# Kernel tuning notes

Measured on AMD Instinct MI355X. Metric: run time of the kernel, lower is better.

Reference implementation:

```python
import jax, jax.numpy as jnp
import numpy as np

EPS_RMS = 1.1920929e-07  # torch.finfo(float32).eps, RMSNorm default when eps=None
EPS_BN = 1e-5            # BatchNorm1d default eps
NUM_CODES = 4096
EMBED_DIM = 64


def rms_norm(x):
    # nn.RMSNorm(embed_dim, elementwise_affine=False)
    ms = jnp.mean(x * x, axis=-1, keepdims=True)
    return x * jax.lax.rsqrt(ms + EPS_RMS)


def get_codebook(codebook_weight, bn_weight, bn_bias):
    # BatchNorm1d with track_running_stats=False: batch stats over codebook rows
    mean = jnp.mean(codebook_weight, axis=0)
    var = jnp.var(codebook_weight, axis=0)  # biased variance, as torch BN uses
    h = (codebook_weight - mean) * jax.lax.rsqrt(var + EPS_BN) * bn_weight + bn_bias
    return rms_norm(h)


def setup_inputs() -> dict:
    key = jax.random.key(0)
    k1, k2 = jax.random.split(key)
    z = jax.random.normal(k1, (8, 4096, EMBED_DIM), dtype=jnp.float32)
    # codebook init: uniform(-1/num_codes, 1/num_codes)
    codebook_weight = jax.random.uniform(
        k2, (NUM_CODES, EMBED_DIM), dtype=jnp.float32,
        minval=-1.0 / NUM_CODES, maxval=1.0 / NUM_CODES)
    bn_weight = jnp.ones((EMBED_DIM,), dtype=jnp.float32)
    bn_bias = jnp.zeros((EMBED_DIM,), dtype=jnp.float32)
    return {"z": z, "codebook_weight": codebook_weight,
            "bn_weight": bn_weight, "bn_bias": bn_bias}


def reference(z, codebook_weight, bn_weight, bn_bias):
    # c_in / c_out are Identity since width == embed_dim
    z_e = rms_norm(z)                                   # [B, S, D]
    cb = get_codebook(codebook_weight, bn_weight, bn_bias)  # [K, D]

    z_flat = z_e.reshape(-1, z_e.shape[-1])             # [N, D]
    # argmin of cdist == argmin of squared distance (sqrt is monotone)
    d2 = (jnp.sum(z_flat * z_flat, axis=1, keepdims=True)
          - 2.0 * (z_flat @ cb.T)
          + jnp.sum(cb * cb, axis=1))                   # [N, K]
    q = jnp.argmin(d2, axis=1)                          # [N]

    z_q = cb[q].reshape(z_e.shape)                      # gather codes
    q = q.reshape(z_e.shape[:-1])

    # straight-through: gradient flows to z_e only
    z_q_st = z_e + jax.lax.stop_gradient(z_q - z_e)
    # ret_dict entries: 'z' (detached z_e), 'q', 'z_q' (detached)
    return (z_q_st, jax.lax.stop_gradient(z_e), q, jax.lax.stop_gradient(z_q))
```

## Files before the change

### kernel.cpp

```cpp
#include <hip/hip_runtime.h>
#include <math.h>

#define NROWS 32768
#define DIM   64
#define NCODE 4096
#define EPS_RMS 1.1920929e-07f
#define EPS_BN  1e-5f

typedef _Float16 f16x8 __attribute__((ext_vector_type(8)));
typedef float    f32x4 __attribute__((ext_vector_type(4)));

#define WS_PS   0
#define WS_PQ   16384
#define WS_CC   32768
#define WS_CB32 49152
#define WS_PH   (49152 + 1048576)
#define WS_PL   (WS_PH + 524288)

#define OUT1 ((size_t)NROWS * DIM)
#define OUT2 ((size_t)2 * NROWS * DIM)
#define OUT3 (OUT2 + NROWS)

#define MFMA16(a, b, c) __builtin_amdgcn_mfma_f32_16x16x32_f16(a, b, c, 0, 0, 0)

__global__ __launch_bounds__(256) void k_bn1(const float* __restrict__ w,
                                             char* __restrict__ wsb) {
    __shared__ float s1[4][64], s2[4][64];
    int lane = threadIdx.x & 63, v = threadIdx.x >> 6;
    long base = (long)blockIdx.x * 64 + v * 16;
    float s = 0.f, sq = 0.f;
    #pragma unroll
    for (int i = 0; i < 16; i++) {
        float x = w[(base + i) * DIM + lane];
        s += x; sq += x * x;
    }
    s1[v][lane] = s; s2[v][lane] = sq;
    __syncthreads();
    if (threadIdx.x < 64) {
        float ts = s1[0][lane] + s1[1][lane] + s1[2][lane] + s1[3][lane];
        float tq = s2[0][lane] + s2[1][lane] + s2[2][lane] + s2[3][lane];
        ((float*)(wsb + WS_PS))[blockIdx.x * 64 + lane] = ts;
        ((float*)(wsb + WS_PQ))[blockIdx.x * 64 + lane] = tq;
    }
}

__global__ __launch_bounds__(256) void k_cb(const float* __restrict__ w,
                                            const float* __restrict__ bnw,
                                            const float* __restrict__ bnb,
                                            char* __restrict__ wsb) {
    __shared__ float s1[4][64], s2[4][64], af[64], bf[64];
    __shared__ _Float16 sh[16][64], sl[16][64];
    int t = threadIdx.x, lane = t & 63, v = t >> 6;
    const float* ps = (const float*)(wsb + WS_PS);
    const float* pq = (const float*)(wsb + WS_PQ);
    float s = 0.f, sq = 0.f;
    #pragma unroll
    for (int b = 0; b < 16; b++) {
        s  += ps[(v * 16 + b) * 64 + lane];
        sq += pq[(v * 16 + b) * 64 + lane];
    }
    s1[v][lane] = s; s2[v][lane] = sq;
    __syncthreads();
    if (t < 64) {
        float ts = s1[0][lane] + s1[1][lane] + s1[2][lane] + s1[3][lane];
        float tq = s2[0][lane] + s2[1][lane] + s2[2][lane] + s2[3][lane];
        float mean = ts * (1.0f / NCODE);
        float var  = tq * (1.0f / NCODE) - mean * mean;
        float a = rsqrtf(var + EPS_BN) * bnw[lane];
        af[lane] = a;
        bf[lane] = bnb[lane] - mean * a;
    }
    __syncthreads();
    float a = af[lane], bb = bf[lane];
    float* cb32 = (float*)(wsb + WS_CB32);
    float* ccp  = (float*)(wsb + WS_CC);
    int g = blockIdx.x;
    #pragma unroll
    for (int i = 0; i < 4; i++) {
        int  rl  = v * 4 + i;
        long row = (long)g * 16 + rl;
        float x = w[row * DIM + lane];
        float h = fmaf(x, a, bb);
        float ss = h * h;
        #pragma unroll
        for (int m = 1; m < 64; m <<= 1) ss += __shfl_xor(ss, m);
        float rms = rsqrtf(ss * (1.0f / DIM) + EPS_RMS);
        float c = h * rms;
        cb32[row * DIM + lane] = c;
        _Float16 ch = (_Float16)c;
        sh[rl][lane] = ch;
        sl[rl][lane] = (_Float16)(c - (float)ch);
        float cs = c * c;
        #pragma unroll
        for (int m = 1; m < 64; m <<= 1) cs += __shfl_xor(cs, m);
        if (lane == 0) ccp[row] = -0.5f * cs;
    }
    __syncthreads();
    {
        int u = t & 127;
        int c = u >> 6, l = u & 63;
        int codel = l & 15;
        int kbase = c * 32 + (l >> 4) * 8;
        size_t dst = (size_t)((g * 2 + c) * 64 + l) * 16;
        if (t < 128) {
            *(f16x8*)(wsb + WS_PH + dst) = *(const f16x8*)&sh[codel][kbase];
        } else {
            *(f16x8*)(wsb + WS_PL + dst) = *(const f16x8*)&sl[codel][kbase];
        }
    }
}

__global__ __launch_bounds__(256, 3) void k_main(const float* __restrict__ z,
                                                 const char* __restrict__ wsb,
                                                 float* __restrict__ out) {
    __shared__ __align__(16) unsigned char sm[18688];

    const int tid  = threadIdx.x;
    const int lane = tid & 63;
    const int w    = tid >> 6;
    const int l15  = lane & 15;
    const int l4   = lane >> 4;
    const long rowbase = (long)blockIdx.x * 64;

    const float* ccnG = (const float*)(wsb + WS_CC);
    const float* cb32 = (const float*)(wsb + WS_CB32);

    {
        int r = tid >> 2, seg = tid & 3;
        const float4* zp = (const float4*)(z + (rowbase + r) * DIM + seg * 16);
        float4 v4[4];
        float ss = 0.f;
        #pragma unroll
        for (int i = 0; i < 4; i++) {
            v4[i] = zp[i];
            ss += v4[i].x * v4[i].x + v4[i].y * v4[i].y + v4[i].z * v4[i].z + v4[i].w * v4[i].w;
        }
        ss += __shfl_xor(ss, 1);
        ss += __shfl_xor(ss, 2);
        float rms = rsqrtf(ss * (1.0f / DIM) + EPS_RMS);
        float4* oz = (float4*)(out + OUT1 + (rowbase + r) * DIM + seg * 16);
        __align__(16) _Float16 hb[16], lb[16];
        #pragma unroll
        for (int i = 0; i < 4; i++) {
            float xs[4] = {v4[i].x, v4[i].y, v4[i].z, v4[i].w};
            #pragma unroll
            for (int j = 0; j < 4; j++) {
                float x = xs[j] * rms;
                _Float16 h = (_Float16)x;
                hb[i * 4 + j] = h;
                lb[i * 4 + j] = (_Float16)(x - (float)h);
                xs[j] = x;
            }
            oz[i] = make_float4(xs[0], xs[1], xs[2], xs[3]);
        }
        unsigned char* zhp = sm + r * 128 + seg * 32;
        ((f16x8*)zhp)[0] = ((f16x8*)hb)[0];
        ((f16x8*)zhp)[1] = ((f16x8*)hb)[1];
        unsigned char* zlp = zhp + 8192;
        ((f16x8*)zlp)[0] = ((f16x8*)lb)[0];
        ((f16x8*)zlp)[1] = ((f16x8*)lb)[1];
    }
    __syncthreads();

    f16x8 ah[4][2], al[4][2];
    #pragma unroll
    for (int s = 0; s < 4; s++)
        #pragma unroll
        for (int c = 0; c < 2; c++) {
            int off = (s * 16 + l15) * 128 + c * 64 + l4 * 16;
            ah[s][c] = *(const f16x8*)(sm + off);
            al[s][c] = *(const f16x8*)(sm + 8192 + off);
        }

    float bmax[4][4];
    int   bix[4][4];
    #pragma unroll
    for (int s = 0; s < 4; s++)
        #pragma unroll
        for (int r = 0; r < 4; r++) { bmax[s][r] = -3.4e38f; bix[s][r] = 0; }

    const int gw = w * 64;
    const char* pH = wsb + WS_PH + (size_t)(gw * 2) * 1024 + lane * 16;
    const char* pL = wsb + WS_PL + (size_t)(gw * 2) * 1024 + lane * 16;
    const float* cn = ccnG + gw * 16 + l15;

    #define LOADB(H0, H1, L0, L1, CC, k)                       \
        H0 = *(const f16x8*)(pH + (size_t)(k) * 2048);         \
        H1 = *(const f16x8*)(pH + (size_t)(k) * 2048 + 1024);  \
        L0 = *(const f16x8*)(pL + (size_t)(k) * 2048);         \
        L1 = *(const f16x8*)(pL + (size_t)(k) * 2048 + 1024);  \
        CC = cn[(k) * 16];

    #define COMPUTE(H0, H1, L0, L1, CC, k)                                        \
    {                                                                             \
        int code = (gw + (k)) * 16 + l15;                                         \
        _Pragma("unroll")                                                         \
        for (int s = 0; s < 4; s++) {                                             \
            f32x4 a2 = {CC, CC, CC, CC};                                          \
            a2 = MFMA16(ah[s][0], H0, a2);                                        \
            a2 = MFMA16(ah[s][1], H1, a2);                                        \
            a2 = MFMA16(ah[s][0], L0, a2);                                        \
            a2 = MFMA16(ah[s][1], L1, a2);                                        \
            a2 = MFMA16(al[s][0], H0, a2);                                        \
            a2 = MFMA16(al[s][1], H1, a2);                                        \
            _Pragma("unroll")                                                     \
            for (int r = 0; r < 4; r++) {                                         \
                if (a2[r] > bmax[s][r]) { bmax[s][r] = a2[r]; bix[s][r] = code; } \
            }                                                                     \
        }                                                                         \
    }

    f16x8 hA0, hA1, lA0, lA1, hB0, hB1, lB0, lB1;
    float ccA, ccB;
    LOADB(hA0, hA1, lA0, lA1, ccA, 0);
    #pragma unroll 1
    for (int k = 0; k < 62; k += 2) {
        LOADB(hB0, hB1, lB0, lB1, ccB, k + 1);
        COMPUTE(hA0, hA1, lA0, lA1, ccA, k);
        LOADB(hA0, hA1, lA0, lA1, ccA, k + 2);
        COMPUTE(hB0, hB1, lB0, lB1, ccB, k + 1);
    }
    LOADB(hB0, hB1, lB0, lB1, ccB, 63);
    COMPUTE(hA0, hA1, lA0, lA1, ccA, 62);
    COMPUTE(hB0, hB1, lB0, lB1, ccB, 63);

    float* redd = (float*)(sm + 16384);
    int*   redi = (int*)(sm + 17408);
    int*   bidx = (int*)(sm + 18432);
    #pragma unroll
    for (int s = 0; s < 4; s++)
        #pragma unroll
        for (int r = 0; r < 4; r++) {
            float d = bmax[s][r];
            int   ix = bix[s][r];
            #pragma unroll
            for (int m = 1; m < 16; m <<= 1) {
                float od = __shfl_xor(d, m);
                int   oi = __shfl_xor(ix, m);
                if (od > d || (od == d && oi < ix)) { d = od; ix = oi; }
            }
            if (l15 == 0) {
                int row = s * 16 + l4 * 4 + r;
                redd[row * 4 + w] = d;
                redi[row * 4 + w] = ix;
            }
        }
    __syncthreads();
    if (tid < 64) {
        float bv = redd[tid * 4];
        int   bi_ = redi[tid * 4];
        #pragma unroll
        for (int j = 1; j < 4; j++) {
            float dj = redd[tid * 4 + j];
            int   ij = redi[tid * 4 + j];
            if (dj > bv || (dj == bv && ij < bi_)) { bv = dj; bi_ = ij; }
        }
        bidx[tid] = bi_;
        out[OUT2 + rowbase + tid] = (float)bi_;
    }
    __syncthreads();
    {
        int r = tid >> 2, seg = tid & 3;
        int ix = bidx[r];
        const float4* src = (const float4*)(cb32 + (long)ix * DIM + seg * 16);
        float4* o0 = (float4*)(out + (rowbase + r) * DIM + seg * 16);
        float4* o3 = (float4*)(out + OUT3 + (rowbase + r) * DIM + seg * 16);
        #pragma unroll
        for (int i = 0; i < 4; i++) { float4 t4 = src[i]; o0[i] = t4; o3[i] = t4; }
    }
}

extern "C" void kernel_launch(void* const* d_in, const int* in_sizes, int n_in,
                              void* d_out, int out_size, void* d_ws, size_t ws_size,
                              hipStream_t stream) {
    const float* z   = (const float*)d_in[0];
    const float* w   = (const float*)d_in[1];
    const float* bnw = (const float*)d_in[2];
    const float* bnb = (const float*)d_in[3];
    float* out = (float*)d_out;
    char*  wsb = (char*)d_ws;

    k_bn1 <<<64,  256, 0, stream>>>(w, wsb);
    k_cb  <<<256, 256, 0, stream>>>(w, bnw, bnb, wsb);
    k_main<<<512, 256, 0, stream>>>(z, wsb, out);
}
```

Measured before the change: 70.26 us.

## Split codebook search across two blocks per row tile and merge in final kernel

The main kernel now launches twice as many blocks, and each block scans half of the codebook for its 64 rows. It writes per-row partial best score and index to workspace, and a new k_final kernel merges the two halves, gathers the code vectors and writes the outputs. Launch bounds raise the occupancy target from 3 to 4 blocks per CU. The aim is more parallelism across 256 CUs, at the cost of computing the z normalization twice, an extra kernel launch and a workspace round-trip.

```diff
diff --git a/kernel.cpp b/kernel.cpp
--- a/kernel.cpp
+++ b/kernel.cpp
@@ -16,6 +16,7 @@
 #define WS_CB32 49152
 #define WS_PH   (49152 + 1048576)
 #define WS_PL   (WS_PH + 524288)
+#define WS_PART (WS_PL + 524288)
 
 #define OUT1 ((size_t)NROWS * DIM)
 #define OUT2 ((size_t)2 * NROWS * DIM)
@@ -110,20 +111,21 @@
     }
 }
 
-__global__ __launch_bounds__(256, 3) void k_main(const float* __restrict__ z,
-                                                 const char* __restrict__ wsb,
+__global__ __launch_bounds__(256, 4) void k_main(const float* __restrict__ z,
+                                                 char* __restrict__ wsb,
                                                  float* __restrict__ out) {
-    __shared__ __align__(16) unsigned char sm[18688];
+    __shared__ __align__(16) unsigned char sm[18432];
 
     const int tid  = threadIdx.x;
     const int lane = tid & 63;
     const int w    = tid >> 6;
     const int l15  = lane & 15;
     const int l4   = lane >> 4;
-    const long rowbase = (long)blockIdx.x * 64;
+    const int rowblk = blockIdx.x >> 1;
+    const int half   = blockIdx.x & 1;
+    const long rowbase = (long)rowblk * 64;
 
     const float* ccnG = (const float*)(wsb + WS_CC);
-    const float* cb32 = (const float*)(wsb + WS_CB32);
 
     {
         int r = tid >> 2, seg = tid & 3;
@@ -151,7 +153,7 @@
                 lb[i * 4 + j] = (_Float16)(x - (float)h);
                 xs[j] = x;
             }
-            oz[i] = make_float4(xs[0], xs[1], xs[2], xs[3]);
+            if (half == 0) oz[i] = make_float4(xs[0], xs[1], xs[2], xs[3]);
         }
         unsigned char* zhp = sm + r * 128 + seg * 32;
         ((f16x8*)zhp)[0] = ((f16x8*)hb)[0];
@@ -179,7 +181,7 @@
         #pragma unroll
         for (int r = 0; r < 4; r++) { bmax[s][r] = -3.4e38f; bix[s][r] = 0; }
 
-    const int gw = w * 64;
+    const int gw = half * 128 + w * 32;
     const char* pH = wsb + WS_PH + (size_t)(gw * 2) * 1024 + lane * 16;
     const char* pL = wsb + WS_PL + (size_t)(gw * 2) * 1024 + lane * 16;
     const float* cn = ccnG + gw * 16 + l15;
@@ -214,19 +216,18 @@
     float ccA, ccB;
     LOADB(hA0, hA1, lA0, lA1, ccA, 0);
     #pragma unroll 1
-    for (int k = 0; k < 62; k += 2) {
+    for (int k = 0; k < 30; k += 2) {
         LOADB(hB0, hB1, lB0, lB1, ccB, k + 1);
         COMPUTE(hA0, hA1, lA0, lA1, ccA, k);
         LOADB(hA0, hA1, lA0, lA1, ccA, k + 2);
         COMPUTE(hB0, hB1, lB0, lB1, ccB, k + 1);
     }
-    LOADB(hB0, hB1, lB0, lB1, ccB, 63);
-    COMPUTE(hA0, hA1, lA0, lA1, ccA, 62);
-    COMPUTE(hB0, hB1, lB0, lB1, ccB, 63);
+    LOADB(hB0, hB1, lB0, lB1, ccB, 31);
+    COMPUTE(hA0, hA1, lA0, lA1, ccA, 30);
+    COMPUTE(hB0, hB1, lB0, lB1, ccB, 31);
 
     float* redd = (float*)(sm + 16384);
     int*   redi = (int*)(sm + 17408);
-    int*   bidx = (int*)(sm + 18432);
     #pragma unroll
     for (int s = 0; s < 4; s++)
         #pragma unroll
@@ -255,19 +256,30 @@
             int   ij = redi[tid * 4 + j];
             if (dj > bv || (dj == bv && ij < bi_)) { bv = dj; bi_ = ij; }
         }
-        bidx[tid] = bi_;
-        out[OUT2 + rowbase + tid] = (float)bi_;
-    }
-    __syncthreads();
-    {
-        int r = tid >> 2, seg = tid & 3;
-        int ix = bidx[r];
-        const float4* src = (const float4*)(cb32 + (long)ix * DIM + seg * 16);
-        float4* o0 = (float4*)(out + (rowbase + r) * DIM + seg * 16);
-        float4* o3 = (float4*)(out + OUT3 + (rowbase + r) * DIM + seg * 16);
-        #pragma unroll
-        for (int i = 0; i < 4; i++) { float4 t4 = src[i]; o0[i] = t4; o3[i] = t4; }
-    }
+        float* part = (float*)(wsb + WS_PART);
+        size_t off = ((size_t)half * NROWS + rowbase + tid) * 2;
+        part[off]     = bv;
+        part[off + 1] = (float)bi_;
+    }
+}
+
+__global__ __launch_bounds__(256) void k_final(const char* __restrict__ wsb,
+                                               float* __restrict__ out) {
+    int gid = blockIdx.x * 256 + threadIdx.x;
+    int r   = gid >> 3;
+    int seg = gid & 7;
+    const float* part = (const float*)(wsb + WS_PART);
+    const float* cb32 = (const float*)(wsb + WS_CB32);
+    float d0 = part[(size_t)r * 2],           i0f = part[(size_t)r * 2 + 1];
+    float d1 = part[((size_t)NROWS + r) * 2], i1f = part[((size_t)NROWS + r) * 2 + 1];
+    int i0 = (int)i0f, i1 = (int)i1f;
+    int best = (d1 > d0 || (d1 == d0 && i1 < i0)) ? i1 : i0;
+    const float4* src = (const float4*)(cb32 + (long)best * DIM + seg * 8);
+    float4* o0 = (float4*)(out + (size_t)r * DIM + seg * 8);
+    float4* o3 = (float4*)(out + OUT3 + (size_t)r * DIM + seg * 8);
+    #pragma unroll
+    for (int i = 0; i < 2; i++) { float4 t4 = src[i]; o0[i] = t4; o3[i] = t4; }
+    if (seg == 0) out[OUT2 + r] = (float)best;
 }
 
 extern "C" void kernel_launch(void* const* d_in, const int* in_sizes, int n_in,
@@ -280,7 +292,8 @@
     float* out = (float*)d_out;
     char*  wsb = (char*)d_ws;
 
-    k_bn1 <<<64,  256, 0, stream>>>(w, wsb);
-    k_cb  <<<256, 256, 0, stream>>>(w, bnw, bnb, wsb);
-    k_main<<<512, 256, 0, stream>>>(z, wsb, out);
-}
+    k_bn1  <<<64,   256, 0, stream>>>(w, wsb);
+    k_cb   <<<256,  256, 0, stream>>>(w, bnw, bnb, wsb);
+    k_main <<<1024, 256, 0, stream>>>(z, wsb, out);
+    k_final<<<NROWS * 8 / 256, 256, 0, stream>>>(wsb, out);
+}
```

New measurement: 209.8 us. 199% more time.

## Stage codebook tiles in LDS via async global_load_lds with double buffering

Applied to the files above, without the earlier changes.

Each block now handles 128 rows with 512 threads instead of 64 rows with 256 threads. The packed fp16 hi/lo codebook is streamed through a double-buffered LDS ring using global_load_lds. Each 128-code chunk is shared by all 8 waves, which split the work into 4 row groups by 2 code halves, instead of every wave streaming its own codes from global/L2 directly. This aims to cut redundant codebook traffic. In exchange it uses 96KB of LDS and adds a barrier per chunk, which limits occupancy and adds sync overhead.

```diff
diff --git a/kernel.cpp b/kernel.cpp
--- a/kernel.cpp
+++ b/kernel.cpp
@@ -22,6 +22,12 @@
 #define OUT3 (OUT2 + NROWS)
 
 #define MFMA16(a, b, c) __builtin_amdgcn_mfma_f32_16x16x32_f16(a, b, c, 0, 0, 0)
+
+__device__ __forceinline__ void gload16(void* lds, const void* g) {
+    __builtin_amdgcn_global_load_lds(
+        (const __attribute__((address_space(1))) unsigned int*)g,
+        (__attribute__((address_space(3))) unsigned int*)lds, 16, 0, 0);
+}
 
 __global__ __launch_bounds__(256) void k_bn1(const float* __restrict__ w,
                                              char* __restrict__ wsb) {
@@ -110,20 +116,37 @@
     }
 }
 
-__global__ __launch_bounds__(256, 3) void k_main(const float* __restrict__ z,
-                                                 const char* __restrict__ wsb,
+__global__ __launch_bounds__(512, 2) void k_main(const float* __restrict__ z,
+                                                 char* __restrict__ wsb,
                                                  float* __restrict__ out) {
-    __shared__ __align__(16) unsigned char sm[18688];
+    __shared__ __align__(16) unsigned char sm[98304];
 
     const int tid  = threadIdx.x;
     const int lane = tid & 63;
     const int w    = tid >> 6;
+    const int rg   = w & 3;
+    const int ch   = w >> 2;
     const int l15  = lane & 15;
     const int l4   = lane >> 4;
-    const long rowbase = (long)blockIdx.x * 64;
+    const long rowbase = (long)blockIdx.x * 128;
 
     const float* ccnG = (const float*)(wsb + WS_CC);
     const float* cb32 = (const float*)(wsb + WS_CB32);
+
+    const char* pH = wsb + WS_PH + w * 1024 + lane * 16;
+    const char* pL = wsb + WS_PL + w * 1024 + lane * 16;
+
+    #define STAGE(p, bufoff)                                                \
+    {                                                                       \
+        const char* gh = pH + (size_t)(p) * 16384;                          \
+        const char* gl = pL + (size_t)(p) * 16384;                          \
+        gload16(sm + (bufoff) + w * 1024,          gh);                     \
+        gload16(sm + (bufoff) + 8192 + w * 1024,   gh + 8192);              \
+        gload16(sm + (bufoff) + 16384 + w * 1024,  gl);                     \
+        gload16(sm + (bufoff) + 24576 + w * 1024,  gl + 8192);              \
+    }
+
+    STAGE(0, 0);
 
     {
         int r = tid >> 2, seg = tid & 3;
@@ -153,82 +176,89 @@
             }
             oz[i] = make_float4(xs[0], xs[1], xs[2], xs[3]);
         }
-        unsigned char* zhp = sm + r * 128 + seg * 32;
+        unsigned char* zhp = sm + 65536 + r * 128 + seg * 32;
         ((f16x8*)zhp)[0] = ((f16x8*)hb)[0];
         ((f16x8*)zhp)[1] = ((f16x8*)hb)[1];
-        unsigned char* zlp = zhp + 8192;
+        unsigned char* zlp = zhp + 16384;
         ((f16x8*)zlp)[0] = ((f16x8*)lb)[0];
         ((f16x8*)zlp)[1] = ((f16x8*)lb)[1];
     }
     __syncthreads();
 
-    f16x8 ah[4][2], al[4][2];
-    #pragma unroll
-    for (int s = 0; s < 4; s++)
+    f16x8 ah[2][2], al[2][2];
+    #pragma unroll
+    for (int s = 0; s < 2; s++)
         #pragma unroll
         for (int c = 0; c < 2; c++) {
-            int off = (s * 16 + l15) * 128 + c * 64 + l4 * 16;
+            int off = 65536 + (rg * 32 + s * 16 + l15) * 128 + c * 64 + l4 * 16;
             ah[s][c] = *(const f16x8*)(sm + off);
-            al[s][c] = *(const f16x8*)(sm + 8192 + off);
-        }
-
-    float bmax[4][4];
-    int   bix[4][4];
-    #pragma unroll
-    for (int s = 0; s < 4; s++)
+            al[s][c] = *(const f16x8*)(sm + 16384 + off);
+        }
+
+    float bmax[2][4];
+    int   bix[2][4];
+    #pragma unroll
+    for (int s = 0; s < 2; s++)
         #pragma unroll
         for (int r = 0; r < 4; r++) { bmax[s][r] = -3.4e38f; bix[s][r] = 0; }
 
-    const int gw = w * 64;
-    const char* pH = wsb + WS_PH + (size_t)(gw * 2) * 1024 + lane * 16;
-    const char* pL = wsb + WS_PL + (size_t)(gw * 2) * 1024 + lane * 16;
-    const float* cn = ccnG + gw * 16 + l15;
-
-    #define LOADB(H0, H1, L0, L1, CC, k)                       \
-        H0 = *(const f16x8*)(pH + (size_t)(k) * 2048);         \
-        H1 = *(const f16x8*)(pH + (size_t)(k) * 2048 + 1024);  \
-        L0 = *(const f16x8*)(pL + (size_t)(k) * 2048);         \
-        L1 = *(const f16x8*)(pL + (size_t)(k) * 2048 + 1024);  \
-        CC = cn[(k) * 16];
-
-    #define COMPUTE(H0, H1, L0, L1, CC, k)                                        \
-    {                                                                             \
-        int code = (gw + (k)) * 16 + l15;                                         \
-        _Pragma("unroll")                                                         \
-        for (int s = 0; s < 4; s++) {                                             \
-            f32x4 a2 = {CC, CC, CC, CC};                                          \
-            a2 = MFMA16(ah[s][0], H0, a2);                                        \
-            a2 = MFMA16(ah[s][1], H1, a2);                                        \
-            a2 = MFMA16(ah[s][0], L0, a2);                                        \
-            a2 = MFMA16(ah[s][1], L1, a2);                                        \
-            a2 = MFMA16(al[s][0], H0, a2);                                        \
-            a2 = MFMA16(al[s][1], H1, a2);                                        \
-            _Pragma("unroll")                                                     \
-            for (int r = 0; r < 4; r++) {                                         \
-                if (a2[r] > bmax[s][r]) { bmax[s][r] = a2[r]; bix[s][r] = code; } \
-            }                                                                     \
-        }                                                                         \
-    }
-
-    f16x8 hA0, hA1, lA0, lA1, hB0, hB1, lB0, lB1;
-    float ccA, ccB;
-    LOADB(hA0, hA1, lA0, lA1, ccA, 0);
+    float ccv[4];
+    #pragma unroll
+    for (int q = 0; q < 4; q++)
+        ccv[q] = ccnG[ch * 64 + q * 16 + l15];
+
+    #define COMPUTE(p, bufoff)                                                     \
+    {                                                                              \
+        _Pragma("unroll")                                                          \
+        for (int q = 0; q < 4; q++) {                                              \
+            f16x8 bh[2], bl[2];                                                    \
+            _Pragma("unroll")                                                      \
+            for (int c = 0; c < 2; c++) {                                          \
+                int boff = (bufoff) + (ch * 8 + q * 2 + c) * 1024 + lane * 16;     \
+                bh[c] = *(const f16x8*)(sm + boff);                                \
+                bl[c] = *(const f16x8*)(sm + 16384 + boff);                        \
+            }                                                                      \
+            int code = (p) * 128 + ch * 64 + q * 16 + l15;                         \
+            _Pragma("unroll")                                                      \
+            for (int s = 0; s < 2; s++) {                                          \
+                f32x4 a2 = {ccv[q], ccv[q], ccv[q], ccv[q]};                       \
+                a2 = MFMA16(ah[s][0], bh[0], a2);                                  \
+                a2 = MFMA16(ah[s][1], bh[1], a2);                                  \
+                a2 = MFMA16(ah[s][0], bl[0], a2);                                  \
+                a2 = MFMA16(ah[s][1], bl[1], a2);                                  \
+                a2 = MFMA16(al[s][0], bh[0], a2);                                  \
+                a2 = MFMA16(al[s][1], bh[1], a2);                                  \
+                _Pragma("unroll")                                                  \
+                for (int r = 0; r < 4; r++) {                                      \
+                    if (a2[r] > bmax[s][r]) { bmax[s][r] = a2[r]; bix[s][r] = code; } \
+                }                                                                  \
+            }                                                                      \
+        }                                                                          \
+    }
+
     #pragma unroll 1
-    for (int k = 0; k < 62; k += 2) {
-        LOADB(hB0, hB1, lB0, lB1, ccB, k + 1);
-        COMPUTE(hA0, hA1, lA0, lA1, ccA, k);
-        LOADB(hA0, hA1, lA0, lA1, ccA, k + 2);
-        COMPUTE(hB0, hB1, lB0, lB1, ccB, k + 1);
-    }
-    LOADB(hB0, hB1, lB0, lB1, ccB, 63);
-    COMPUTE(hA0, hA1, lA0, lA1, ccA, 62);
-    COMPUTE(hB0, hB1, lB0, lB1, ccB, 63);
-
-    float* redd = (float*)(sm + 16384);
-    int*   redi = (int*)(sm + 17408);
-    int*   bidx = (int*)(sm + 18432);
-    #pragma unroll
-    for (int s = 0; s < 4; s++)
+    for (int p = 0; p < 31; ++p) {
+        STAGE(p + 1, ((p + 1) & 1) * 32768);
+        float ccn_nx[4];
+        {
+            const float* cn = ccnG + (p + 1) * 128 + ch * 64 + l15;
+            #pragma unroll
+            for (int q = 0; q < 4; q++) ccn_nx[q] = cn[q * 16];
+        }
+
+        COMPUTE(p, (p & 1) * 32768);
+
+        __syncthreads();
+        #pragma unroll
+        for (int q = 0; q < 4; q++) ccv[q] = ccn_nx[q];
+    }
+    COMPUTE(31, 32768);
+
+    float* redd = (float*)sm;
+    int*   redi = (int*)(sm + 1024);
+    int*   bidx = (int*)(sm + 2048);
+    #pragma unroll
+    for (int s = 0; s < 2; s++)
         #pragma unroll
         for (int r = 0; r < 4; r++) {
             float d = bmax[s][r];
@@ -240,21 +270,19 @@
                 if (od > d || (od == d && oi < ix)) { d = od; ix = oi; }
             }
             if (l15 == 0) {
-                int row = s * 16 + l4 * 4 + r;
-                redd[row * 4 + w] = d;
-                redi[row * 4 + w] = ix;
+                int row = rg * 32 + s * 16 + l4 * 4 + r;
+                redd[row * 2 + ch] = d;
+                redi[row * 2 + ch] = ix;
             }
         }
     __syncthreads();
-    if (tid < 64) {
-        float bv = redd[tid * 4];
-        int   bi_ = redi[tid * 4];
-        #pragma unroll
-        for (int j = 1; j < 4; j++) {
-            float dj = redd[tid * 4 + j];
-            int   ij = redi[tid * 4 + j];
-            if (dj > bv || (dj == bv && ij < bi_)) { bv = dj; bi_ = ij; }
-        }
+    if (tid < 128) {
+        float d0 = redd[tid * 2 + 0];
+        int   i0 = redi[tid * 2 + 0];
+        float d1 = redd[tid * 2 + 1];
+        int   i1 = redi[tid * 2 + 1];
+        float bv = d0; int bi_ = i0;
+        if (d1 > bv || (d1 == bv && i1 < bi_)) { bv = d1; bi_ = i1; }
         bidx[tid] = bi_;
         out[OUT2 + rowbase + tid] = (float)bi_;
     }
@@ -282,5 +310,5 @@
 
     k_bn1 <<<64,  256, 0, stream>>>(w, wsb);
     k_cb  <<<256, 256, 0, stream>>>(w, bnw, bnb, wsb);
-    k_main<<<512, 256, 0, stream>>>(z, wsb, out);
-}
+    k_main<<<256, 512, 0, stream>>>(z, wsb, out);
+}
```

Result: slower. 75.88 us (+8.0%).

## Switch nearest-code search from 16x16x32 to 32x32x16 MFMA tiles

Applied to the files above, without the earlier changes.

Moves the split-fp16 distance GEMM from 16x16x32 MFMA to 32x32x16 MFMA. Each wave now handles 32-code tiles across two 32-row slabs, and the packed codebook layout written by the prep kernel is changed to match the new B-operand lane mapping. Larger tiles mean fewer B-operand loads and fewer argmin compare passes per MFMA FLOP. In exchange it uses more accumulator and bmax/bix registers, so launch bounds drop from 3 to 2 blocks per CU, and the cross-lane reduction grows to 32 lanes with a new row mapping.

```diff
diff --git a/kernel.cpp b/kernel.cpp
--- a/kernel.cpp
+++ b/kernel.cpp
@@ -7,8 +7,8 @@
 #define EPS_RMS 1.1920929e-07f
 #define EPS_BN  1e-5f
 
-typedef _Float16 f16x8 __attribute__((ext_vector_type(8)));
-typedef float    f32x4 __attribute__((ext_vector_type(4)));
+typedef _Float16 f16x8  __attribute__((ext_vector_type(8)));
+typedef float    f32x16 __attribute__((ext_vector_type(16)));
 
 #define WS_PS   0
 #define WS_PQ   16384
@@ -21,7 +21,7 @@
 #define OUT2 ((size_t)2 * NROWS * DIM)
 #define OUT3 (OUT2 + NROWS)
 
-#define MFMA16(a, b, c) __builtin_amdgcn_mfma_f32_16x16x32_f16(a, b, c, 0, 0, 0)
+#define MFMA32(a, b, c) __builtin_amdgcn_mfma_f32_32x32x16_f16(a, b, c, 0, 0, 0)
 
 __global__ __launch_bounds__(256) void k_bn1(const float* __restrict__ w,
                                              char* __restrict__ wsb) {
@@ -97,29 +97,29 @@
     }
     __syncthreads();
     {
-        int u = t & 127;
-        int c = u >> 6, l = u & 63;
-        int codel = l & 15;
-        int kbase = c * 32 + (l >> 4) * 8;
-        size_t dst = (size_t)((g * 2 + c) * 64 + l) * 16;
-        if (t < 128) {
-            *(f16x8*)(wsb + WS_PH + dst) = *(const f16x8*)&sh[codel][kbase];
-        } else {
-            *(f16x8*)(wsb + WS_PL + dst) = *(const f16x8*)&sl[codel][kbase];
-        }
-    }
-}
-
-__global__ __launch_bounds__(256, 3) void k_main(const float* __restrict__ z,
-                                                 const char* __restrict__ wsb,
+        int m  = t >> 7;
+        int v2 = t & 127;
+        int p  = v2 & 1;
+        int c  = (v2 >> 1) & 3;
+        int cl = v2 >> 3;
+        int lane32 = (g & 1) * 16 + cl + 32 * p;
+        size_t dst = (((size_t)(g >> 1) * 4 + c) * 64 + lane32) * 16;
+        const _Float16* src = (m == 0) ? &sh[cl][c * 16 + p * 8] : &sl[cl][c * 16 + p * 8];
+        char* base = wsb + (m == 0 ? WS_PH : WS_PL);
+        *(f16x8*)(base + dst) = *(const f16x8*)src;
+    }
+}
+
+__global__ __launch_bounds__(256, 2) void k_main(const float* __restrict__ z,
+                                                 char* __restrict__ wsb,
                                                  float* __restrict__ out) {
     __shared__ __align__(16) unsigned char sm[18688];
 
     const int tid  = threadIdx.x;
     const int lane = tid & 63;
-    const int w    = tid >> 6;
-    const int l15  = lane & 15;
-    const int l4   = lane >> 4;
+    const int q    = tid >> 6;
+    const int l31  = lane & 31;
+    const int l5   = lane >> 5;
     const long rowbase = (long)blockIdx.x * 64;
 
     const float* ccnG = (const float*)(wsb + WS_CC);
@@ -162,87 +162,99 @@
     }
     __syncthreads();
 
-    f16x8 ah[4][2], al[4][2];
-    #pragma unroll
-    for (int s = 0; s < 4; s++)
-        #pragma unroll
-        for (int c = 0; c < 2; c++) {
-            int off = (s * 16 + l15) * 128 + c * 64 + l4 * 16;
-            ah[s][c] = *(const f16x8*)(sm + off);
-            al[s][c] = *(const f16x8*)(sm + 8192 + off);
-        }
-
-    float bmax[4][4];
-    int   bix[4][4];
-    #pragma unroll
-    for (int s = 0; s < 4; s++)
-        #pragma unroll
-        for (int r = 0; r < 4; r++) { bmax[s][r] = -3.4e38f; bix[s][r] = 0; }
-
-    const int gw = w * 64;
-    const char* pH = wsb + WS_PH + (size_t)(gw * 2) * 1024 + lane * 16;
-    const char* pL = wsb + WS_PL + (size_t)(gw * 2) * 1024 + lane * 16;
-    const float* cn = ccnG + gw * 16 + l15;
-
-    #define LOADB(H0, H1, L0, L1, CC, k)                       \
-        H0 = *(const f16x8*)(pH + (size_t)(k) * 2048);         \
-        H1 = *(const f16x8*)(pH + (size_t)(k) * 2048 + 1024);  \
-        L0 = *(const f16x8*)(pL + (size_t)(k) * 2048);         \
-        L1 = *(const f16x8*)(pL + (size_t)(k) * 2048 + 1024);  \
-        CC = cn[(k) * 16];
-
-    #define COMPUTE(H0, H1, L0, L1, CC, k)                                        \
-    {                                                                             \
-        int code = (gw + (k)) * 16 + l15;                                         \
-        _Pragma("unroll")                                                         \
-        for (int s = 0; s < 4; s++) {                                             \
-            f32x4 a2 = {CC, CC, CC, CC};                                          \
-            a2 = MFMA16(ah[s][0], H0, a2);                                        \
-            a2 = MFMA16(ah[s][1], H1, a2);                                        \
-            a2 = MFMA16(ah[s][0], L0, a2);                                        \
-            a2 = MFMA16(ah[s][1], L1, a2);                                        \
-            a2 = MFMA16(al[s][0], H0, a2);                                        \
-            a2 = MFMA16(al[s][1], H1, a2);                                        \
-            _Pragma("unroll")                                                     \
-            for (int r = 0; r < 4; r++) {                                         \
-                if (a2[r] > bmax[s][r]) { bmax[s][r] = a2[r]; bix[s][r] = code; } \
-            }                                                                     \
-        }                                                                         \
-    }
-
-    f16x8 hA0, hA1, lA0, lA1, hB0, hB1, lB0, lB1;
+    f16x8 ahh[2][4], ahl[2][4];
+    #pragma unroll
+    for (int s = 0; s < 2; s++)
+        #pragma unroll
+        for (int c = 0; c < 4; c++) {
+            int off = (s * 32 + l31) * 128 + c * 32 + l5 * 16;
+            ahh[s][c] = *(const f16x8*)(sm + off);
+            ahl[s][c] = *(const f16x8*)(sm + 8192 + off);
+        }
+
+    float bmax[2][16];
+    int   bix[2][16];
+    #pragma unroll
+    for (int s = 0; s < 2; s++)
+        #pragma unroll
+        for (int r = 0; r < 16; r++) { bmax[s][r] = -3.4e38f; bix[s][r] = 0; }
+
+    const int qcode = q * 1024;
+    const char* pHq = wsb + WS_PH + (size_t)q * 131072 + lane * 16;
+    const char* pLq = wsb + WS_PL + (size_t)q * 131072 + lane * 16;
+    const float* ccq = ccnG + qcode + l31;
+
+    #define LOADB(BH, BL, CCV, t)                                       \
+        BH[0] = *(const f16x8*)(pHq + (size_t)(t) * 4096);              \
+        BH[1] = *(const f16x8*)(pHq + (size_t)(t) * 4096 + 1024);       \
+        BH[2] = *(const f16x8*)(pHq + (size_t)(t) * 4096 + 2048);       \
+        BH[3] = *(const f16x8*)(pHq + (size_t)(t) * 4096 + 3072);       \
+        BL[0] = *(const f16x8*)(pLq + (size_t)(t) * 4096);              \
+        BL[1] = *(const f16x8*)(pLq + (size_t)(t) * 4096 + 1024);       \
+        BL[2] = *(const f16x8*)(pLq + (size_t)(t) * 4096 + 2048);       \
+        BL[3] = *(const f16x8*)(pLq + (size_t)(t) * 4096 + 3072);       \
+        CCV = ccq[(t) * 32];
+
+    #define COMPUTE(BH, BL, CCV, t)                                                \
+    {                                                                              \
+        int code = qcode + (t) * 32 + l31;                                         \
+        _Pragma("unroll")                                                          \
+        for (int s = 0; s < 2; s++) {                                              \
+            f32x16 a2;                                                             \
+            _Pragma("unroll")                                                      \
+            for (int r = 0; r < 16; r++) a2[r] = CCV;                              \
+            a2 = MFMA32(ahh[s][0], BH[0], a2);                                     \
+            a2 = MFMA32(ahh[s][1], BH[1], a2);                                     \
+            a2 = MFMA32(ahh[s][2], BH[2], a2);                                     \
+            a2 = MFMA32(ahh[s][3], BH[3], a2);                                     \
+            a2 = MFMA32(ahh[s][0], BL[0], a2);                                     \
+            a2 = MFMA32(ahh[s][1], BL[1], a2);                                     \
+            a2 = MFMA32(ahh[s][2], BL[2], a2);                                     \
+            a2 = MFMA32(ahh[s][3], BL[3], a2);                                     \
+            a2 = MFMA32(ahl[s][0], BH[0], a2);                                     \
+            a2 = MFMA32(ahl[s][1], BH[1], a2);                                     \
+            a2 = MFMA32(ahl[s][2], BH[2], a2);                                     \
+            a2 = MFMA32(ahl[s][3], BH[3], a2);                                     \
+            _Pragma("unroll")                                                      \
+            for (int r = 0; r < 16; r++) {                                         \
+                if (a2[r] > bmax[s][r]) { bmax[s][r] = a2[r]; bix[s][r] = code; }  \
+            }                                                                      \
+        }                                                                          \
+    }
+
+    f16x8 bhA[4], blA[4], bhB[4], blB[4];
     float ccA, ccB;
-    LOADB(hA0, hA1, lA0, lA1, ccA, 0);
+    LOADB(bhA, blA, ccA, 0);
     #pragma unroll 1
-    for (int k = 0; k < 62; k += 2) {
-        LOADB(hB0, hB1, lB0, lB1, ccB, k + 1);
-        COMPUTE(hA0, hA1, lA0, lA1, ccA, k);
-        LOADB(hA0, hA1, lA0, lA1, ccA, k + 2);
-        COMPUTE(hB0, hB1, lB0, lB1, ccB, k + 1);
-    }
-    LOADB(hB0, hB1, lB0, lB1, ccB, 63);
-    COMPUTE(hA0, hA1, lA0, lA1, ccA, 62);
-    COMPUTE(hB0, hB1, lB0, lB1, ccB, 63);
+    for (int t = 0; t < 30; t += 2) {
+        LOADB(bhB, blB, ccB, t + 1);
+        COMPUTE(bhA, blA, ccA, t);
+        LOADB(bhA, blA, ccA, t + 2);
+        COMPUTE(bhB, blB, ccB, t + 1);
+    }
+    LOADB(bhB, blB, ccB, 31);
+    COMPUTE(bhA, blA, ccA, 30);
+    COMPUTE(bhB, blB, ccB, 31);
 
     float* redd = (float*)(sm + 16384);
     int*   redi = (int*)(sm + 17408);
     int*   bidx = (int*)(sm + 18432);
     #pragma unroll
-    for (int s = 0; s < 4; s++)
-        #pragma unroll
-        for (int r = 0; r < 4; r++) {
+    for (int s = 0; s < 2; s++)
+        #pragma unroll
+        for (int r = 0; r < 16; r++) {
             float d = bmax[s][r];
             int   ix = bix[s][r];
             #pragma unroll
-            for (int m = 1; m < 16; m <<= 1) {
+            for (int m = 1; m < 32; m <<= 1) {
                 float od = __shfl_xor(d, m);
                 int   oi = __shfl_xor(ix, m);
                 if (od > d || (od == d && oi < ix)) { d = od; ix = oi; }
             }
-            if (l15 == 0) {
-                int row = s * 16 + l4 * 4 + r;
-                redd[row * 4 + w] = d;
-                redi[row * 4 + w] = ix;
+            if (l31 == 0) {
+                int row = s * 32 + (r & 3) + 8 * (r >> 2) + 4 * l5;
+                redd[row * 4 + q] = d;
+                redi[row * 4 + q] = ix;
             }
         }
     __syncthreads();
```

Result: slower. 86.71 us (+23.4%).
